# Kernel tuning notes

Hardware: AMD Instinct MI355X
Metric: run time of the kernel (lower is better)

## Reference

```python
import jax, jax.numpy as jnp
import numpy as np

B = 64        # graphs
N = 2048      # nodes per graph (equal-sized graphs -> regular top-k)
D = 128       # in_channels
RATIO = 0.5
E = 4_194_304 # edges (avg degree 32)
K = int(np.ceil(RATIO * N))  # nodes kept per graph = 1024


def setup_inputs() -> dict:
    key = jax.random.key(0)
    k1, k2, k3 = jax.random.split(key, 3)
    x = jax.random.normal(k1, (B * N, D), dtype=jnp.float32)
    edge_index = jax.random.randint(k2, (2, E), 0, B * N, dtype=jnp.int32)
    batch = jnp.repeat(jnp.arange(B, dtype=jnp.int32), N)  # node i -> graph i//N
    w = jax.random.normal(k3, (D,), dtype=jnp.float32)     # TopKPooling scoring weight
    return {"x": x, "edge_index": edge_index, "batch": batch, "w": w}


def reference(x, edge_index, batch, w):
    # PyG TopKPooling: score = nonlinearity((x . w) / ||w||), default nonlinearity = tanh
    score = jnp.tanh((x @ w) / jnp.linalg.norm(w))               # [B*N]
    # per-graph top-k (graphs are equal-sized -> reshape + lax.top_k)
    top_vals, top_idx = jax.lax.top_k(score.reshape(B, N), K)    # [B, K] each
    offsets = (jnp.arange(B, dtype=top_idx.dtype) * N)[:, None]
    perm = (top_idx + offsets).reshape(-1)                       # [B*K] global node ids
    score_sel = top_vals.reshape(-1)                             # [B*K]
    # gate selected node features by their score
    x_out = x[perm] * score_sel[:, None]                         # [B*K, D]
    # relabel nodes: old id -> new compacted id, -1 if dropped
    new_idx = jnp.full((B * N,), -1, dtype=jnp.int32).at[perm].set(
        jnp.arange(B * K, dtype=jnp.int32))
    nr = new_idx[edge_index[0]]
    nc = new_idx[edge_index[1]]
    edge_mask = (nr >= 0) & (nc >= 0)                            # [E] kept edges
    edge_index_out = jnp.where(edge_mask, jnp.stack([nr, nc]), 0)  # fixed-shape, masked
    batch_out = jnp.repeat(jnp.arange(B, dtype=jnp.int32), K)
    return x_out, edge_index_out, batch_out, perm, score_sel, edge_mask
```

## Files before the change

### kernel.cpp

```cpp
#include <hip/hip_runtime.h>
#include <math.h>

#define BG 64
#define NN 2048
#define DD 128
#define KK 1024
#define EE 4194304

#define OFF_EI   8388608
#define OFF_BAT  16777216
#define OFF_PERM 16842752
#define OFF_SCR  16908288
#define OFF_MSK  16973824

#define EDGE_BLOCKS   256
#define GATHER_BLOCKS 512
#define SORT_BLOCKS   256

typedef unsigned long long u64;
typedef float f4v __attribute__((ext_vector_type(4)));
typedef int   i4v __attribute__((ext_vector_type(4)));

__device__ __forceinline__ void nt_store4(float a, float b, float c, float d, float* p) {
    f4v v = {a, b, c, d};
    __builtin_nontemporal_store(v, (f4v*)p);
}

__global__ __launch_bounds__(256) void score_kernel(
    const float2* __restrict__ x2, const float2* __restrict__ w2,
    float* __restrict__ scores)
{
    int node = (blockIdx.x * 256 + threadIdx.x) >> 6;
    int lane = threadIdx.x & 63;
    float2 xv = x2[(size_t)node * 64 + lane];
    float2 wv = w2[lane];
    float dot = xv.x * wv.x + xv.y * wv.y;
    float ww  = wv.x * wv.x + wv.y * wv.y;
    #pragma unroll
    for (int off = 32; off >= 1; off >>= 1) {
        dot += __shfl_xor(dot, off);
        ww  += __shfl_xor(ww, off);
    }
    if (lane == 0) scores[node] = tanhf(dot / sqrtf(ww));
}

__device__ __forceinline__ unsigned ford(float f) {
    unsigned b = __float_as_uint(f);
    return (b & 0x80000000u) ? ~b : (b | 0x80000000u);
}
__device__ __forceinline__ float forddec(unsigned u) {
    unsigned b = (u & 0x80000000u) ? (u & 0x7FFFFFFFu) : ~u;
    return __uint_as_float(b);
}

__device__ __forceinline__ u64 regswap(u64 v, int elem_idx, int j, int k) {
    u64 p = __shfl_xor(v, j, 64);
    bool dir   = ((elem_idx & k) == 0);
    bool lower = ((elem_idx & j) == 0);
    return (dir == lower) ? (v > p ? v : p) : (v < p ? v : p);
}

__global__ __launch_bounds__(1024) void sort_kernel(
    const float* __restrict__ scores, const int* __restrict__ ei,
    int* __restrict__ perm_int, unsigned short* __restrict__ tab16,
    unsigned* __restrict__ maskbits,
    float* __restrict__ out_batch, float* __restrict__ out_perm,
    float* __restrict__ out_score)
{
    const int b = blockIdx.x;
    const int t = threadIdx.x;

    if (b >= BG) {
        const i4v* e4 = (const i4v*)ei;
        const size_t total4 = 2 * EE / 4;
        size_t tid = (size_t)(b - BG) * 1024 + t;
        int acc = 0;
        for (size_t i = tid; i < total4; i += (size_t)(SORT_BLOCKS - BG) * 1024) {
            i4v v = e4[i];
            acc ^= v[0] ^ v[1] ^ v[2] ^ v[3];
        }
        asm volatile("" :: "v"(acc));
        return;
    }

    __shared__ u64 keys[NN];
    __shared__ unsigned mw[NN / 32];

    float s0 = scores[b * NN + t];
    float s1 = scores[b * NN + 1024 + t];
    u64 va = ((u64)ford(s0) << 32) | (unsigned)(NN - 1 - t);
    u64 vb = ((u64)ford(s1) << 32) | (unsigned)(NN - 1 - (1024 + t));

    #pragma unroll
    for (int k = 2; k <= 64; k <<= 1)
        #pragma unroll
        for (int j = k >> 1; j >= 1; j >>= 1) {
            va = regswap(va, t, j, k);
            vb = regswap(vb, 1024 + t, j, k);
        }

    keys[t] = va; keys[1024 + t] = vb;
    if (t < NN / 32) mw[t] = 0u;
    __syncthreads();

    for (int k = 128; k <= 2048; k <<= 1) {
        for (int j = k >> 1; j >= 64; j >>= 1) {
            int i = ((t & ~(j - 1)) << 1) | (t & (j - 1));
            int p = i | j;
            u64 A = keys[i], C = keys[p];
            bool sw = ((i & k) == 0) ? (A < C) : (A > C);
            if (sw) { keys[i] = C; keys[p] = A; }
            __syncthreads();
        }
        va = keys[t]; vb = keys[1024 + t];
        #pragma unroll
        for (int j = 32; j >= 1; j >>= 1) {
            va = regswap(va, t, j, k);
            vb = regswap(vb, 1024 + t, j, k);
        }
        if (k < 2048) {
            keys[t] = va; keys[1024 + t] = vb;
            __syncthreads();
        }
    }

    int idx  = NN - 1 - (int)(va & 0xFFFFFFFFu);
    float s  = forddec((unsigned)(va >> 32));
    int gid  = b * NN + idx;
    int row  = b * KK + t;
    perm_int[row]  = gid;
    tab16[gid]     = (unsigned short)row;
    out_perm[row]  = (float)gid;
    out_score[row] = s;
    out_batch[row] = (float)b;
    atomicOr(&mw[idx >> 5], 1u << (idx & 31));
    __syncthreads();
    if (t < NN / 32) maskbits[b * (NN / 32) + t] = mw[t];
}

__global__ __launch_bounds__(1024) void tail_kernel(
    const int* __restrict__ e0, const int* __restrict__ e1,
    const unsigned* __restrict__ mb, const unsigned short* __restrict__ tab,
    const float4* __restrict__ x4, const int* __restrict__ perm_int,
    const float* __restrict__ out_score, float* __restrict__ out)
{
    __shared__ unsigned smask[BG * NN / 32];
    int bid = blockIdx.x;
    int t   = threadIdx.x;
    if (bid < EDGE_BLOCKS) {
        ((uint4*)smask)[t] = ((const uint4*)mb)[t];
        __syncthreads();

        float* oe0 = out + OFF_EI;
        float* oe1 = out + OFF_EI + EE;
        float* om  = out + OFF_MSK;

        size_t eb = (size_t)bid * 4096 + t;
        i4v r[4], c[4];
        #pragma unroll
        for (int u = 0; u < 4; ++u) {
            r[u] = ((const i4v*)e0)[eb + u * 1024];
            c[u] = ((const i4v*)e1)[eb + u * 1024];
        }
        #pragma unroll
        for (int u = 0; u < 4; ++u) {
            size_t i = eb + u * 1024;
            float er[4], ec[4], em[4];
            #pragma unroll
            for (int q = 0; q < 4; ++q) {
                int rq = r[u][q], cq = c[u][q];
                unsigned m = (smask[(unsigned)rq >> 5] >> (rq & 31)) &
                             (smask[(unsigned)cq >> 5] >> (cq & 31)) & 1u;
                float nr = 0.0f, nc = 0.0f;
                if (m) {
                    nr = (float)tab[rq];
                    nc = (float)tab[cq];
                }
                er[q] = nr; ec[q] = nc; em[q] = m ? 1.0f : 0.0f;
            }
            nt_store4(er[0], er[1], er[2], er[3], oe0 + 4 * i);
            nt_store4(ec[0], ec[1], ec[2], ec[3], oe1 + 4 * i);
            nt_store4(em[0], em[1], em[2], em[3], om  + 4 * i);
        }
    } else {
        int gb   = bid - EDGE_BLOCKS;
        int lane = t & 31;
        int grp  = t >> 5;
        int rbase = gb * 128 + grp;
        int g[4]; float s[4];
        #pragma unroll
        for (int p = 0; p < 4; ++p) {
            int row = rbase + p * 32;
            g[p] = perm_int[row];
            s[p] = out_score[row];
        }
        float4 v[4];
        #pragma unroll
        for (int p = 0; p < 4; ++p)
            v[p] = x4[(size_t)g[p] * 32 + lane];
        #pragma unroll
        for (int p = 0; p < 4; ++p) {
            int row = rbase + p * 32;
            nt_store4(v[p].x * s[p], v[p].y * s[p], v[p].z * s[p], v[p].w * s[p],
                      out + ((size_t)row * 32 + lane) * 4);
        }
    }
}

extern "C" void kernel_launch(void* const* d_in, const int* in_sizes, int n_in,
                              void* d_out, int out_size, void* d_ws, size_t ws_size,
                              hipStream_t stream)
{
    const float* x  = (const float*)d_in[0];
    const int*   ei = (const int*)d_in[1];
    const float* w  = (const float*)d_in[3];
    float* out = (float*)d_out;

    float*          scores   = (float*)d_ws;
    int*            perm_i   = (int*)d_ws + BG * NN;
    unsigned short* tab16    = (unsigned short*)((char*)d_ws + (BG * NN + BG * KK) * 4);
    unsigned*       maskbits = (unsigned*)((char*)d_ws + (BG * NN + BG * KK) * 4 + BG * NN * 2);

    score_kernel<<<BG * NN / 4, 256, 0, stream>>>(
        (const float2*)x, (const float2*)w, scores);

    sort_kernel<<<SORT_BLOCKS, 1024, 0, stream>>>(
        scores, ei, perm_i, tab16, maskbits,
        out + OFF_BAT, out + OFF_PERM, out + OFF_SCR);

    tail_kernel<<<EDGE_BLOCKS + GATHER_BLOCKS, 1024, 0, stream>>>(
        ei, ei + EE, maskbits, tab16,
        (const float4*)x, perm_i, out + OFF_SCR, out);
}
```

Before: 64.81 us.

## Fuse sort and tail kernels with per-graph flags for intra-kernel overlap

Merges the sort kernel and the edge/gather tail kernel into one launch. Sort blocks publish per-graph ready flags and a global done counter with release atomics. Gather blocks spin only on their own graph's flag, while edge blocks prefetch their edge indices with nontemporal loads before waiting for all sorts to finish. This removes a kernel boundary and the old edge-index cache warm-up, letting gather and edge loads overlap the sort. In exchange it adds a memset launch and depends on forward-progress spinning, which could deadlock if sort blocks are not scheduled before the waiting blocks.

```diff
diff --git a/kernel.cpp b/kernel.cpp
--- a/kernel.cpp
+++ b/kernel.cpp
@@ -13,9 +13,10 @@
 #define OFF_SCR  16908288
 #define OFF_MSK  16973824
 
-#define EDGE_BLOCKS   256
-#define GATHER_BLOCKS 512
-#define SORT_BLOCKS   256
+#define SORT_BLK 64
+#define EDGE_BLK 256
+#define GATH_BLK 512
+#define NBLK (SORT_BLK + EDGE_BLK + GATH_BLK)
 
 typedef unsigned long long u64;
 typedef float f4v __attribute__((ext_vector_type(4)));
@@ -60,108 +61,105 @@
     return (dir == lower) ? (v > p ? v : p) : (v < p ? v : p);
 }
 
-__global__ __launch_bounds__(1024) void sort_kernel(
+__global__ __launch_bounds__(1024) void fused2_kernel(
     const float* __restrict__ scores, const int* __restrict__ ei,
+    const float4* __restrict__ x4,
     int* __restrict__ perm_int, unsigned short* __restrict__ tab16,
-    unsigned* __restrict__ maskbits,
-    float* __restrict__ out_batch, float* __restrict__ out_perm,
-    float* __restrict__ out_score)
+    unsigned* __restrict__ maskbits, int* __restrict__ flags,
+    float* __restrict__ out)
 {
-    const int b = blockIdx.x;
-    const int t = threadIdx.x;
-
-    if (b >= BG) {
-        const i4v* e4 = (const i4v*)ei;
-        const size_t total4 = 2 * EE / 4;
-        size_t tid = (size_t)(b - BG) * 1024 + t;
-        int acc = 0;
-        for (size_t i = tid; i < total4; i += (size_t)(SORT_BLOCKS - BG) * 1024) {
-            i4v v = e4[i];
-            acc ^= v[0] ^ v[1] ^ v[2] ^ v[3];
-        }
-        asm volatile("" :: "v"(acc));
-        return;
-    }
-
-    __shared__ u64 keys[NN];
-    __shared__ unsigned mw[NN / 32];
-
-    float s0 = scores[b * NN + t];
-    float s1 = scores[b * NN + 1024 + t];
-    u64 va = ((u64)ford(s0) << 32) | (unsigned)(NN - 1 - t);
-    u64 vb = ((u64)ford(s1) << 32) | (unsigned)(NN - 1 - (1024 + t));
-
-    #pragma unroll
-    for (int k = 2; k <= 64; k <<= 1)
-        #pragma unroll
-        for (int j = k >> 1; j >= 1; j >>= 1) {
-            va = regswap(va, t, j, k);
-            vb = regswap(vb, 1024 + t, j, k);
-        }
-
-    keys[t] = va; keys[1024 + t] = vb;
-    if (t < NN / 32) mw[t] = 0u;
-    __syncthreads();
-
-    for (int k = 128; k <= 2048; k <<= 1) {
-        for (int j = k >> 1; j >= 64; j >>= 1) {
-            int i = ((t & ~(j - 1)) << 1) | (t & (j - 1));
-            int p = i | j;
-            u64 A = keys[i], C = keys[p];
-            bool sw = ((i & k) == 0) ? (A < C) : (A > C);
-            if (sw) { keys[i] = C; keys[p] = A; }
-            __syncthreads();
-        }
-        va = keys[t]; vb = keys[1024 + t];
-        #pragma unroll
-        for (int j = 32; j >= 1; j >>= 1) {
-            va = regswap(va, t, j, k);
-            vb = regswap(vb, 1024 + t, j, k);
-        }
-        if (k < 2048) {
-            keys[t] = va; keys[1024 + t] = vb;
-            __syncthreads();
-        }
-    }
-
-    int idx  = NN - 1 - (int)(va & 0xFFFFFFFFu);
-    float s  = forddec((unsigned)(va >> 32));
-    int gid  = b * NN + idx;
-    int row  = b * KK + t;
-    perm_int[row]  = gid;
-    tab16[gid]     = (unsigned short)row;
-    out_perm[row]  = (float)gid;
-    out_score[row] = s;
-    out_batch[row] = (float)b;
-    atomicOr(&mw[idx >> 5], 1u << (idx & 31));
-    __syncthreads();
-    if (t < NN / 32) maskbits[b * (NN / 32) + t] = mw[t];
-}
-
-__global__ __launch_bounds__(1024) void tail_kernel(
-    const int* __restrict__ e0, const int* __restrict__ e1,
-    const unsigned* __restrict__ mb, const unsigned short* __restrict__ tab,
-    const float4* __restrict__ x4, const int* __restrict__ perm_int,
-    const float* __restrict__ out_score, float* __restrict__ out)
-{
-    __shared__ unsigned smask[BG * NN / 32];
-    int bid = blockIdx.x;
-    int t   = threadIdx.x;
-    if (bid < EDGE_BLOCKS) {
-        ((uint4*)smask)[t] = ((const uint4*)mb)[t];
+    __shared__ u64 shbuf[NN + 32];
+    const int bid = blockIdx.x;
+    const int t   = threadIdx.x;
+    int* done = flags + BG;
+
+    if (bid < SORT_BLK) {
+        u64* keys = shbuf;
+        unsigned* mw = (unsigned*)(shbuf + NN);
+        const int b = bid;
+
+        float s0 = scores[b * NN + t];
+        float s1 = scores[b * NN + 1024 + t];
+        u64 va = ((u64)ford(s0) << 32) | (unsigned)(NN - 1 - t);
+        u64 vb = ((u64)ford(s1) << 32) | (unsigned)(NN - 1 - (1024 + t));
+
+        #pragma unroll
+        for (int k = 2; k <= 64; k <<= 1)
+            #pragma unroll
+            for (int j = k >> 1; j >= 1; j >>= 1) {
+                va = regswap(va, t, j, k);
+                vb = regswap(vb, 1024 + t, j, k);
+            }
+
+        keys[t] = va; keys[1024 + t] = vb;
+        if (t < NN / 32) mw[t] = 0u;
+        __syncthreads();
+
+        for (int k = 128; k <= 2048; k <<= 1) {
+            for (int j = k >> 1; j >= 64; j >>= 1) {
+                int i = ((t & ~(j - 1)) << 1) | (t & (j - 1));
+                int p = i | j;
+                u64 A = keys[i], C = keys[p];
+                bool sw = ((i & k) == 0) ? (A < C) : (A > C);
+                if (sw) { keys[i] = C; keys[p] = A; }
+                __syncthreads();
+            }
+            va = keys[t]; vb = keys[1024 + t];
+            #pragma unroll
+            for (int j = 32; j >= 1; j >>= 1) {
+                va = regswap(va, t, j, k);
+                vb = regswap(vb, 1024 + t, j, k);
+            }
+            if (k < 2048) {
+                keys[t] = va; keys[1024 + t] = vb;
+                __syncthreads();
+            }
+        }
+
+        int idx  = NN - 1 - (int)(va & 0xFFFFFFFFu);
+        float s  = forddec((unsigned)(va >> 32));
+        int gid  = b * NN + idx;
+        int row  = b * KK + t;
+        perm_int[row]        = gid;
+        tab16[gid]           = (unsigned short)row;
+        out[OFF_PERM + row]  = (float)gid;
+        out[OFF_SCR + row]   = s;
+        out[OFF_BAT + row]   = (float)b;
+        atomicOr(&mw[idx >> 5], 1u << (idx & 31));
+        __syncthreads();
+        if (t < NN / 32) maskbits[b * (NN / 32) + t] = mw[t];
+        __syncthreads();
+        if (t == 0) {
+            __threadfence();
+            __hip_atomic_store(&flags[b], 1, __ATOMIC_RELEASE, __HIP_MEMORY_SCOPE_AGENT);
+            __hip_atomic_fetch_add(done, 1, __ATOMIC_RELEASE, __HIP_MEMORY_SCOPE_AGENT);
+        }
+    } else if (bid < SORT_BLK + EDGE_BLK) {
+        const int ebid = bid - SORT_BLK;
+        const i4v* e0 = (const i4v*)ei;
+        const i4v* e1 = (const i4v*)(ei + EE);
+        size_t eb = (size_t)ebid * 4096 + t;
+
+        i4v r[4], c[4];
+        #pragma unroll
+        for (int u = 0; u < 4; ++u) {
+            r[u] = __builtin_nontemporal_load(e0 + eb + u * 1024);
+            c[u] = __builtin_nontemporal_load(e1 + eb + u * 1024);
+        }
+
+        if (t == 0) {
+            while (__hip_atomic_load(done, __ATOMIC_ACQUIRE, __HIP_MEMORY_SCOPE_AGENT) < BG)
+                __builtin_amdgcn_s_sleep(16);
+        }
+        __syncthreads();
+
+        unsigned* smask = (unsigned*)shbuf;
+        ((uint4*)smask)[t] = ((const uint4*)maskbits)[t];
         __syncthreads();
 
         float* oe0 = out + OFF_EI;
         float* oe1 = out + OFF_EI + EE;
         float* om  = out + OFF_MSK;
-
-        size_t eb = (size_t)bid * 4096 + t;
-        i4v r[4], c[4];
-        #pragma unroll
-        for (int u = 0; u < 4; ++u) {
-            r[u] = ((const i4v*)e0)[eb + u * 1024];
-            c[u] = ((const i4v*)e1)[eb + u * 1024];
-        }
         #pragma unroll
         for (int u = 0; u < 4; ++u) {
             size_t i = eb + u * 1024;
@@ -173,8 +171,8 @@
                              (smask[(unsigned)cq >> 5] >> (cq & 31)) & 1u;
                 float nr = 0.0f, nc = 0.0f;
                 if (m) {
-                    nr = (float)tab[rq];
-                    nc = (float)tab[cq];
+                    nr = (float)tab16[rq];
+                    nc = (float)tab16[cq];
                 }
                 er[q] = nr; ec[q] = nc; em[q] = m ? 1.0f : 0.0f;
             }
@@ -183,16 +181,23 @@
             nt_store4(em[0], em[1], em[2], em[3], om  + 4 * i);
         }
     } else {
-        int gb   = bid - EDGE_BLOCKS;
-        int lane = t & 31;
-        int grp  = t >> 5;
-        int rbase = gb * 128 + grp;
+        const int gb    = bid - SORT_BLK - EDGE_BLK;
+        const int graph = gb >> 3;
+        if (t == 0) {
+            while (__hip_atomic_load(&flags[graph], __ATOMIC_ACQUIRE, __HIP_MEMORY_SCOPE_AGENT) == 0)
+                __builtin_amdgcn_s_sleep(16);
+        }
+        __syncthreads();
+
+        const int lane = t & 31;
+        const int grp  = t >> 5;
+        const int rbase = gb * 128 + grp;
         int g[4]; float s[4];
         #pragma unroll
         for (int p = 0; p < 4; ++p) {
             int row = rbase + p * 32;
             g[p] = perm_int[row];
-            s[p] = out_score[row];
+            s[p] = out[OFF_SCR + row];
         }
         float4 v[4];
         #pragma unroll
@@ -216,19 +221,18 @@
     const float* w  = (const float*)d_in[3];
     float* out = (float*)d_out;
 
-    float*          scores   = (float*)d_ws;
-    int*            perm_i   = (int*)d_ws + BG * NN;
-    unsigned short* tab16    = (unsigned short*)((char*)d_ws + (BG * NN + BG * KK) * 4);
-    unsigned*       maskbits = (unsigned*)((char*)d_ws + (BG * NN + BG * KK) * 4 + BG * NN * 2);
+    char* wsb = (char*)d_ws;
+    float*          scores   = (float*)wsb;
+    int*            perm_i   = (int*)(wsb + BG * NN * 4);
+    unsigned short* tab16    = (unsigned short*)(wsb + (BG * NN + BG * KK) * 4);
+    unsigned*       maskbits = (unsigned*)(wsb + (BG * NN + BG * KK) * 4 + BG * NN * 2);
+    int*            flags    = (int*)(wsb + (BG * NN + BG * KK) * 4 + BG * NN * 2 + (BG * NN / 8));
+
+    hipMemsetAsync(flags, 0, (BG + 1) * sizeof(int), stream);
 
     score_kernel<<<BG * NN / 4, 256, 0, stream>>>(
         (const float2*)x, (const float2*)w, scores);
 
-    sort_kernel<<<SORT_BLOCKS, 1024, 0, stream>>>(
-        scores, ei, perm_i, tab16, maskbits,
-        out + OFF_BAT, out + OFF_PERM, out + OFF_SCR);
-
-    tail_kernel<<<EDGE_BLOCKS + GATHER_BLOCKS, 1024, 0, stream>>>(
-        ei, ei + EE, maskbits, tab16,
-        (const float4*)x, perm_i, out + OFF_SCR, out);
-}
+    fused2_kernel<<<NBLK, 1024, 0, stream>>>(
+        scores, ei, (const float4*)x, perm_i, tab16, maskbits, flags, out);
+}
```

Result: slower. 98.27 us (+51.6%).
